# Kernel optimization log

Measured on AMD Instinct MI355X. Metric: run time of the kernel, lower is better.

Reference implementation:

```python
import jax, jax.numpy as jnp
import numpy as np

N, E, D, H = 10000, 50000, 32, 4
DH = D // H  # head dim = 8


def setup_inputs() -> dict:
    key = jax.random.key(0)
    ks = jax.random.split(key, 16)
    f = lambda k, s: jax.random.normal(k, s, dtype=jnp.float32) * 0.1
    return {
        "in_feat":   f(ks[0], (N, D)),
        "query":     f(ks[1], (N, H, DH)),
        "src_key_w": f(ks[2], (E, H, DH, D)),
        "dst_key_w": f(ks[3], (E, H, DH, D)),
        "src_key_b": f(ks[4], (E, H, DH)),
        "dst_key_b": f(ks[5], (E, H, DH)),
        "src_val_w": f(ks[6], (E, H, DH, D)),
        "dst_val_w": f(ks[7], (E, H, DH, D)),
        "src_val_b": f(ks[8], (E, H, DH)),
        "dst_val_b": f(ks[9], (E, H, DH)),
        "node_w":    f(ks[10], (N, D, D)),
        "node_b":    f(ks[11], (N, D)),
        "ln_g":      jnp.ones((D,), jnp.float32),
        "ln_b":      jnp.zeros((D,), jnp.float32),
        "src":       jax.random.randint(ks[14], (E,), 0, N),
        "dst":       jax.random.randint(ks[15], (E,), 0, N),
    }


def _layer_norm(x, g, b, eps=1e-5):
    mu = jnp.mean(x, axis=-1, keepdims=True)
    var = jnp.var(x, axis=-1, keepdims=True)
    return (x - mu) * jax.lax.rsqrt(var + eps) * g + b


def reference(in_feat, query, src_key_w, dst_key_w, src_key_b, dst_key_b,
              src_val_w, dst_val_w, src_val_b, dst_val_b,
              node_w, node_b, ln_g, ln_b, src, dst):
    u = in_feat[src]  # [E, D] gathered src features
    v = in_feat[dst]  # [E, D] gathered dst features
    # edgewise_linear: per-edge weights, K = Wuk@u + buk + Wvk@v + bvk
    K = (jnp.einsum('ehdi,ei->ehd', src_key_w, u) + src_key_b
         + jnp.einsum('ehdi,ei->ehd', dst_key_w, v) + dst_key_b)  # [E,H,DH]
    V = (jnp.einsum('ehdi,ei->ehd', src_val_w, u) + src_val_b
         + jnp.einsum('ehdi,ei->ehd', dst_val_w, v) + dst_val_b)  # [E,H,DH]
    # e_dot_v(KEY, QUERY): score per edge against dst-node query
    score = jnp.einsum('ehd,ehd->eh', K, query[dst])  # [E, H]
    # edge_softmax: segment softmax over edges grouped by dst node
    smax = jax.ops.segment_max(score, dst, num_segments=N)  # [N, H]
    ex = jnp.exp(score - smax[dst])
    ssum = jax.ops.segment_sum(ex, dst, num_segments=N)
    attn = ex / ssum[dst]  # [E, H]
    # weighted values, scatter-sum to dst nodes
    feat = V * attn[..., None]  # [E, H, DH]
    agg = jax.ops.segment_sum(feat, dst, num_segments=N).reshape(N, D)
    # nodewise_linear with per-node weight, then relu
    out = jnp.einsum('noi,ni->no', node_w, agg) + node_b
    out = jax.nn.relu(out)
    out = in_feat + out              # residual
    out = _layer_norm(out, ln_g, ln_b)  # final LayerNorm
    return out, K.reshape(E, D), V.reshape(E, D), attn
```

## Files before the change

kernel.cpp:

```cpp
#include <hip/hip_runtime.h>
#include <hip/hip_bf16.h>
#include <math.h>

#define DD 32
#define HH 4

__device__ __forceinline__ void atomicMaxFloat(float* addr, float val) {
    if (val >= 0.0f) {
        atomicMax((int*)addr, __float_as_int(val));
    } else {
        atomicMin((unsigned int*)addr, __float_as_uint(val));
    }
}

__device__ __forceinline__ void stage1k(const float* __restrict__ g, float* l) {
    const int lane = threadIdx.x & 63;
    __builtin_amdgcn_global_load_lds(
        (const __attribute__((address_space(1))) void*)(g + lane * 4),
        (__attribute__((address_space(3))) void*)l,
        16, 0, 0);
}

__global__ __launch_bounds__(256) void edge_kernel(
    const float* __restrict__ in_feat,
    const float* __restrict__ query,
    const float* __restrict__ skw, const float* __restrict__ dkw,
    const float* __restrict__ skb, const float* __restrict__ dkb,
    const float* __restrict__ svw, const float* __restrict__ dvw,
    const float* __restrict__ svb, const float* __restrict__ dvb,
    const int* __restrict__ src, const int* __restrict__ dst,
    float* __restrict__ Kout,
    float* __restrict__ Vout,
    float* __restrict__ score,
    int E)
{
    __shared__ float lds[4096];

    const int tid  = threadIdx.x;
    const int lane = tid & 63;
    const int wv   = tid >> 6;
    const int r    = tid >> 3;
    const int t    = tid & 7;

    const int e = blockIdx.x;
    if (e >= E) return;

    const int s = src[e];
    const int d = dst[e];

    const float4 u4 = *(const float4*)(in_feat + (size_t)s * DD + t * 4);
    const float4 v4 = *(const float4*)(in_feat + (size_t)d * DD + t * 4);
    const size_t bo = (size_t)e * DD + r;
    const float kb = skb[bo] + dkb[bo];
    const float vb = svb[bo] + dvb[bo];
    const float q  = query[(size_t)d * DD + r];

    const size_t gchunk = (size_t)e * 1024 + (size_t)wv * 256;
    float* ldsw = &lds[wv * 1024];
    stage1k(skw + gchunk, ldsw + 0);
    stage1k(dkw + gchunk, ldsw + 256);
    stage1k(svw + gchunk, ldsw + 512);
    stage1k(dvw + gchunk, ldsw + 768);

    asm volatile("s_waitcnt vmcnt(0)" ::: "memory");

    const int li = lane * 4;
    const float4 a = *(const float4*)(ldsw + 0   + li);
    const float4 b = *(const float4*)(ldsw + 256 + li);
    const float4 c = *(const float4*)(ldsw + 512 + li);
    const float4 g = *(const float4*)(ldsw + 768 + li);

    float pk = a.x * u4.x + a.y * u4.y + a.z * u4.z + a.w * u4.w
             + b.x * v4.x + b.y * v4.y + b.z * v4.z + b.w * v4.w;
    float pv = c.x * u4.x + c.y * u4.y + c.z * u4.z + c.w * u4.w
             + g.x * v4.x + g.y * v4.y + g.z * v4.z + g.w * v4.w;

    #pragma unroll
    for (int m = 1; m <= 4; m <<= 1) {
        pk += __shfl_xor(pk, m);
        pv += __shfl_xor(pv, m);
    }

    const float kval = pk + kb;
    const float vval = pv + vb;
    if (t == 0) {
        Kout[bo] = kval;
        Vout[bo] = vval;
    }

    float prod = kval * q;
    #pragma unroll
    for (int m = 8; m <= 32; m <<= 1) prod += __shfl_xor(prod, m);
    if (lane == 0) {
        score[(size_t)e * HH + wv] = prod;
    }
}

__global__ void init_kernel(float* __restrict__ smax, float* __restrict__ ssum,
                            float* __restrict__ agg, int NH, int ND)
{
    const int i = blockIdx.x * blockDim.x + threadIdx.x;
    if (i < NH) {
        smax[i] = __int_as_float(0xff800000);
        ssum[i] = 0.0f;
    }
    if (i < ND) agg[i] = 0.0f;
}

__global__ void smax_kernel(const float* __restrict__ score,
                            const int* __restrict__ dst,
                            float* __restrict__ smax, int EH)
{
    const int i = blockIdx.x * blockDim.x + threadIdx.x;
    if (i >= EH) return;
    const int e = i >> 2, h = i & 3;
    atomicMaxFloat(&smax[(size_t)dst[e] * HH + h], score[i]);
}

__global__ void esum_kernel(const float* __restrict__ score,
                            const int* __restrict__ dst,
                            const float* __restrict__ smax,
                            float* __restrict__ ex, float* __restrict__ ssum,
                            int EH)
{
    const int i = blockIdx.x * blockDim.x + threadIdx.x;
    if (i >= EH) return;
    const int e = i >> 2, h = i & 3;
    const int d = dst[e];
    const float x = expf(score[i] - smax[(size_t)d * HH + h]);
    ex[i] = x;
    atomicAdd(&ssum[(size_t)d * HH + h], x);
}

__global__ void attn_agg_kernel(const float* __restrict__ ex,
                                const float* __restrict__ ssum,
                                const int* __restrict__ dst,
                                const float* __restrict__ V,
                                float* __restrict__ attn_out,
                                float* __restrict__ agg,
                                int ED)
{
    const int i = blockIdx.x * blockDim.x + threadIdx.x;
    if (i >= ED) return;
    const int e = i >> 5, c = i & 31, h = c >> 3;
    const int d = dst[e];
    const float a = ex[(size_t)e * HH + h] / ssum[(size_t)d * HH + h];
    if ((c & 7) == 0) attn_out[(size_t)e * HH + h] = a;
    atomicAdd(&agg[(size_t)d * DD + c], V[i] * a);
}

__global__ __launch_bounds__(256) void node_kernel(
    const float* __restrict__ in_feat,
    const float* __restrict__ node_w,
    const float* __restrict__ node_b,
    const float* __restrict__ agg,
    const float* __restrict__ ln_g, const float* __restrict__ ln_b,
    float* __restrict__ out, int N)
{
    __shared__ float ys[DD];
    const int n = blockIdx.x;
    if (n >= N) return;
    const int tid = threadIdx.x;
    const int r = tid >> 3, t = tid & 7;

    const float4 a4 = *(const float4*)(agg + (size_t)n * DD + t * 4);
    const float4 w4 = *(const float4*)(node_w + (size_t)n * 1024 + (size_t)r * 32 + t * 4);
    float p = w4.x * a4.x + w4.y * a4.y + w4.z * a4.z + w4.w * a4.w;
    #pragma unroll
    for (int m = 1; m <= 4; m <<= 1) p += __shfl_xor(p, m);
    if (t == 0) {
        float y = p + node_b[(size_t)n * DD + r];
        y = fmaxf(y, 0.0f) + in_feat[(size_t)n * DD + r];
        ys[r] = y;
    }
    __syncthreads();
    if (tid < 64) {
        const float y = (tid < DD) ? ys[tid] : 0.0f;
        float sum = y;
        #pragma unroll
        for (int m = 1; m <= 32; m <<= 1) sum += __shfl_xor(sum, m);
        const float mu = sum * (1.0f / DD);
        const float dy = (tid < DD) ? (y - mu) : 0.0f;
        float s2 = dy * dy;
        #pragma unroll
        for (int m = 1; m <= 32; m <<= 1) s2 += __shfl_xor(s2, m);
        const float var = s2 * (1.0f / DD);
        if (tid < DD) {
            out[(size_t)n * DD + tid] =
                dy * rsqrtf(var + 1e-5f) * ln_g[tid] + ln_b[tid];
        }
    }
}

extern "C" void kernel_launch(void* const* d_in, const int* in_sizes, int n_in,
                              void* d_out, int out_size, void* d_ws, size_t ws_size,
                              hipStream_t stream) {
    const float* in_feat = (const float*)d_in[0];
    const float* query   = (const float*)d_in[1];
    const float* skw     = (const float*)d_in[2];
    const float* dkw     = (const float*)d_in[3];
    const float* skb     = (const float*)d_in[4];
    const float* dkb     = (const float*)d_in[5];
    const float* svw     = (const float*)d_in[6];
    const float* dvw     = (const float*)d_in[7];
    const float* svb     = (const float*)d_in[8];
    const float* dvb     = (const float*)d_in[9];
    const float* node_w  = (const float*)d_in[10];
    const float* node_b  = (const float*)d_in[11];
    const float* ln_g    = (const float*)d_in[12];
    const float* ln_b    = (const float*)d_in[13];
    const int*   src     = (const int*)d_in[14];
    const int*   dst     = (const int*)d_in[15];

    const int N = in_sizes[0] / DD;
    const int E = in_sizes[14];
    const int NH = N * HH, ND = N * DD;
    const int EH = E * HH, ED = E * DD;

    float* out_node = (float*)d_out;
    float* Kout     = out_node + (size_t)N * DD;
    float* Vout     = Kout + (size_t)E * DD;
    float* attn_out = Vout + (size_t)E * DD;

    float* ws    = (float*)d_ws;
    float* score = ws;
    float* ex    = score + EH;
    float* smax  = ex + EH;
    float* ssum  = smax + NH;
    float* agg   = ssum + NH;

    edge_kernel<<<E, 256, 0, stream>>>(in_feat, query, skw, dkw, skb, dkb,
                                       svw, dvw, svb, dvb, src, dst,
                                       Kout, Vout, score, E);
    init_kernel<<<(ND + 255) / 256, 256, 0, stream>>>(smax, ssum, agg, NH, ND);
    smax_kernel<<<(EH + 255) / 256, 256, 0, stream>>>(score, dst, smax, EH);
    esum_kernel<<<(EH + 255) / 256, 256, 0, stream>>>(score, dst, smax, ex, ssum, EH);
    attn_agg_kernel<<<(ED + 255) / 256, 256, 0, stream>>>(ex, ssum, dst, Vout,
                                                          attn_out, agg, ED);
    node_kernel<<<N, 256, 0, stream>>>(in_feat, node_w, node_b, agg,
                                       ln_g, ln_b, out_node, N);
}
```

Before: 182.6 us.

## Process multiple edges per block with double-buffered weight prefetch and fused segment max

Each edge block now handles 16 edges in sequence. It double-buffers the per-edge weight tiles in LDS, issuing the async global-to-LDS loads for the next edge while computing the current one. The segment-max atomic moves into the edge kernel, which removes the separate smax kernel and its reread of scores; init now runs before the edge kernel. This trades many tiny one-edge blocks for fewer longer blocks with deeper in-flight memory traffic per wave. The risks are less total parallelism to hide memory latency and reliance on in-order vmcnt accounting for correctness.

```diff
diff --git a/kernel.cpp b/kernel.cpp
--- a/kernel.cpp
+++ b/kernel.cpp
@@ -4,6 +4,7 @@
 
 #define DD 32
 #define HH 4
+#define EPB 16
 
 __device__ __forceinline__ void atomicMaxFloat(float* addr, float val) {
     if (val >= 0.0f) {
@@ -32,9 +33,10 @@
     float* __restrict__ Kout,
     float* __restrict__ Vout,
     float* __restrict__ score,
+    float* __restrict__ smax,
     int E)
 {
-    __shared__ float lds[4096];
+    __shared__ float lds[8192];
 
     const int tid  = threadIdx.x;
     const int lane = tid & 63;
@@ -42,57 +44,79 @@
     const int r    = tid >> 3;
     const int t    = tid & 7;
 
-    const int e = blockIdx.x;
-    if (e >= E) return;
-
-    const int s = src[e];
-    const int d = dst[e];
-
-    const float4 u4 = *(const float4*)(in_feat + (size_t)s * DD + t * 4);
-    const float4 v4 = *(const float4*)(in_feat + (size_t)d * DD + t * 4);
-    const size_t bo = (size_t)e * DD + r;
-    const float kb = skb[bo] + dkb[bo];
-    const float vb = svb[bo] + dvb[bo];
-    const float q  = query[(size_t)d * DD + r];
-
-    const size_t gchunk = (size_t)e * 1024 + (size_t)wv * 256;
-    float* ldsw = &lds[wv * 1024];
-    stage1k(skw + gchunk, ldsw + 0);
-    stage1k(dkw + gchunk, ldsw + 256);
-    stage1k(svw + gchunk, ldsw + 512);
-    stage1k(dvw + gchunk, ldsw + 768);
-
-    asm volatile("s_waitcnt vmcnt(0)" ::: "memory");
-
-    const int li = lane * 4;
-    const float4 a = *(const float4*)(ldsw + 0   + li);
-    const float4 b = *(const float4*)(ldsw + 256 + li);
-    const float4 c = *(const float4*)(ldsw + 512 + li);
-    const float4 g = *(const float4*)(ldsw + 768 + li);
-
-    float pk = a.x * u4.x + a.y * u4.y + a.z * u4.z + a.w * u4.w
-             + b.x * v4.x + b.y * v4.y + b.z * v4.z + b.w * v4.w;
-    float pv = c.x * u4.x + c.y * u4.y + c.z * u4.z + c.w * u4.w
-             + g.x * v4.x + g.y * v4.y + g.z * v4.z + g.w * v4.w;
-
-    #pragma unroll
-    for (int m = 1; m <= 4; m <<= 1) {
-        pk += __shfl_xor(pk, m);
-        pv += __shfl_xor(pv, m);
-    }
-
-    const float kval = pk + kb;
-    const float vval = pv + vb;
-    if (t == 0) {
-        Kout[bo] = kval;
-        Vout[bo] = vval;
-    }
-
-    float prod = kval * q;
-    #pragma unroll
-    for (int m = 8; m <= 32; m <<= 1) prod += __shfl_xor(prod, m);
-    if (lane == 0) {
-        score[(size_t)e * HH + wv] = prod;
+    const int e0 = blockIdx.x * EPB;
+    if (e0 >= E) return;
+    const int kmax = (E - e0 < EPB) ? (E - e0) : EPB;
+
+    float* ldsw = &lds[wv * 2048];
+
+    int s = src[e0];
+    int d = dst[e0];
+    {
+        const size_t g0 = (size_t)e0 * 1024 + (size_t)wv * 256;
+        stage1k(skw + g0, ldsw + 0);
+        stage1k(dkw + g0, ldsw + 256);
+        stage1k(svw + g0, ldsw + 512);
+        stage1k(dvw + g0, ldsw + 768);
+    }
+
+    for (int k = 0; k < kmax; ++k) {
+        const int e = e0 + k;
+        const int d_cur = d;
+
+        const float4 u4 = *(const float4*)(in_feat + (size_t)s * DD + t * 4);
+        const float4 v4 = *(const float4*)(in_feat + (size_t)d * DD + t * 4);
+        const size_t bo = (size_t)e * DD + r;
+        const float kb = skb[bo] + dkb[bo];
+        const float vb = svb[bo] + dvb[bo];
+        const float q  = query[(size_t)d * DD + r];
+
+        if (k + 1 < kmax) {
+            const int en = e + 1;
+            s = src[en];
+            d = dst[en];
+            const size_t gn = (size_t)en * 1024 + (size_t)wv * 256;
+            float* nb = ldsw + ((k + 1) & 1) * 1024;
+            stage1k(skw + gn, nb + 0);
+            stage1k(dkw + gn, nb + 256);
+            stage1k(svw + gn, nb + 512);
+            stage1k(dvw + gn, nb + 768);
+        }
+
+        asm volatile("s_waitcnt vmcnt(4)" ::: "memory");
+
+        const float* cb = ldsw + (k & 1) * 1024;
+        const int li = lane * 4;
+        const float4 a = *(const float4*)(cb + 0   + li);
+        const float4 b = *(const float4*)(cb + 256 + li);
+        const float4 c = *(const float4*)(cb + 512 + li);
+        const float4 g = *(const float4*)(cb + 768 + li);
+
+        float pk = a.x * u4.x + a.y * u4.y + a.z * u4.z + a.w * u4.w
+                 + b.x * v4.x + b.y * v4.y + b.z * v4.z + b.w * v4.w;
+        float pv = c.x * u4.x + c.y * u4.y + c.z * u4.z + c.w * u4.w
+                 + g.x * v4.x + g.y * v4.y + g.z * v4.z + g.w * v4.w;
+
+        #pragma unroll
+        for (int m = 1; m <= 4; m <<= 1) {
+            pk += __shfl_xor(pk, m);
+            pv += __shfl_xor(pv, m);
+        }
+
+        const float kval = pk + kb;
+        const float vval = pv + vb;
+        if (t == 0) {
+            Kout[bo] = kval;
+            Vout[bo] = vval;
+        }
+
+        float prod = kval * q;
+        #pragma unroll
+        for (int m = 8; m <= 32; m <<= 1) prod += __shfl_xor(prod, m);
+        if (lane == 0) {
+            score[(size_t)e * HH + wv] = prod;
+            atomicMaxFloat(&smax[(size_t)d_cur * HH + wv], prod);
+        }
     }
 }
 
@@ -105,16 +129,6 @@
         ssum[i] = 0.0f;
     }
     if (i < ND) agg[i] = 0.0f;
-}
-
-__global__ void smax_kernel(const float* __restrict__ score,
-                            const int* __restrict__ dst,
-                            float* __restrict__ smax, int EH)
-{
-    const int i = blockIdx.x * blockDim.x + threadIdx.x;
-    if (i >= EH) return;
-    const int e = i >> 2, h = i & 3;
-    atomicMaxFloat(&smax[(size_t)dst[e] * HH + h], score[i]);
 }
 
 __global__ void esum_kernel(const float* __restrict__ score,
@@ -229,11 +243,10 @@
     float* ssum  = smax + NH;
     float* agg   = ssum + NH;
 
-    edge_kernel<<<E, 256, 0, stream>>>(in_feat, query, skw, dkw, skb, dkb,
-                                       svw, dvw, svb, dvb, src, dst,
-                                       Kout, Vout, score, E);
     init_kernel<<<(ND + 255) / 256, 256, 0, stream>>>(smax, ssum, agg, NH, ND);
-    smax_kernel<<<(EH + 255) / 256, 256, 0, stream>>>(score, dst, smax, EH);
+    edge_kernel<<<(E + EPB - 1) / EPB, 256, 0, stream>>>(
+        in_feat, query, skw, dkw, skb, dkb, svw, dvw, svb, dvb, src, dst,
+        Kout, Vout, score, smax, E);
     esum_kernel<<<(EH + 255) / 256, 256, 0, stream>>>(score, dst, smax, ex, ssum, EH);
     attn_agg_kernel<<<(ED + 255) / 256, 256, 0, stream>>>(ex, ssum, dst, Vout,
                                                           attn_out, agg, ED);
```

After: 207.7 us. 1.14x slower.
